# Kernel tuning notes

Hardware: AMD Instinct MI355X
Metric: run time of the kernel (lower is better)

The kernel has to match this reference:

```python
import jax, jax.numpy as jnp
import numpy as np

D_MODEL = 1024
N_HEADS = 16
SEQ = 512  # == max_seq_len; rel-pos bias requires n_token == max_seq_len


def setup_inputs() -> dict:
    key = jax.random.key(0)
    ks = jax.random.split(key, 12)
    B = 16
    x = jax.random.normal(ks[0], (B, SEQ, D_MODEL), dtype=jnp.float32)
    c = jax.random.normal(ks[1], (B, SEQ, 8), dtype=jnp.float32)  # unused by forward
    s = 1.0 / np.sqrt(D_MODEL)
    Wq = jax.random.normal(ks[2], (D_MODEL, D_MODEL), dtype=jnp.float32) * s
    bq = jnp.zeros((D_MODEL,), dtype=jnp.float32)
    Wk = jax.random.normal(ks[3], (D_MODEL, D_MODEL), dtype=jnp.float32) * s
    bk = jnp.zeros((D_MODEL,), dtype=jnp.float32)
    Wv = jax.random.normal(ks[4], (D_MODEL, D_MODEL), dtype=jnp.float32) * s
    bv = jnp.zeros((D_MODEL,), dtype=jnp.float32)
    Wo = jax.random.normal(ks[5], (D_MODEL, D_MODEL), dtype=jnp.float32) * s
    bo = jnp.zeros((D_MODEL,), dtype=jnp.float32)
    # trunc_normal_(std=0.02) approximated by normal*0.02 (values stay small)
    rel_table = jax.random.normal(ks[6], (2 * SEQ - 1, N_HEADS), dtype=jnp.float32) * 0.02
    return {"x": x, "c": c, "Wq": Wq, "bq": bq, "Wk": Wk, "bk": bk,
            "Wv": Wv, "bv": bv, "Wo": Wo, "bo": bo, "rel_table": rel_table}


def reference(x, c, Wq, bq, Wk, bk, Wv, bv, Wo, bo, rel_table):
    # x: [B, S, D]; c is unused in the original forward
    B, S, D = x.shape
    H = N_HEADS
    dk = D // H
    scale = 1.0 / np.sqrt(dk)

    q = (x @ Wq + bq).reshape(B, S, H, dk)
    k = (x @ Wk + bk).reshape(B, S, H, dk)
    v = (x @ Wv + bv).reshape(B, S, H, dk)

    # scores: [B, H, S, S]
    scores = jnp.einsum('bihd,bjhd->bhij', q, k) * scale

    # relative position bias: index[i,j] = i + (S-1-j), values in [0, 2S-2]
    rel_index = jnp.arange(S)[:, None] + jnp.arange(S - 1, -1, -1)[None, :]  # [S,S]
    bias = rel_table[rel_index]            # [S, S, H]
    scores = scores + jnp.transpose(bias, (2, 0, 1))[None]  # [1,H,S,S]

    # causal_mask=False: original adds False * -1e9 == 0, so no mask term
    probs = jax.nn.softmax(scores, axis=-1)

    out = jnp.einsum('bhij,bjhd->bihd', probs, v).reshape(B, S, D)
    return out @ Wo + bo
```

## Files before the change

### kernel.cpp

```cpp
#include <hip/hip_runtime.h>
#include <hip/hip_bf16.h>
#include <stdint.h>

#define D_MODEL 1024
#define NH 16
#define SEQ 512
#define DK 64
#define BATCH 16
#define M_TOT (BATCH*SEQ)

typedef unsigned short u16;
typedef unsigned int u32;
typedef __attribute__((ext_vector_type(8))) __bf16 bf16x8;
typedef __attribute__((ext_vector_type(4))) u16 ushort4v;
typedef __attribute__((ext_vector_type(4))) float f32x4;

static __device__ __forceinline__ u16 f2bf(float f) {
    union { float f; u32 i; } c; c.f = f;
    return (u16)((c.i + 0x8000u) >> 16);
}
static __device__ __forceinline__ void async_copy16(const void* g, void* l) {
    __builtin_amdgcn_global_load_lds(
        (const __attribute__((address_space(1))) u32*)g,
        (__attribute__((address_space(3))) u32*)l, 16, 0, 0);
}

__global__ __launch_bounds__(256) void convert_f32_bf16(const float* __restrict__ in,
                                                        u16* __restrict__ out) {
    const int i = (blockIdx.x * 256 + threadIdx.x) * 4;
    float4 v = *(const float4*)&in[i];
    ushort4v o;
    o[0] = f2bf(v.x); o[1] = f2bf(v.y); o[2] = f2bf(v.z); o[3] = f2bf(v.w);
    *(ushort4v*)&out[i] = o;
}

__global__ __launch_bounds__(256) void transpose_w3(const float* __restrict__ W0,
                                                    const float* __restrict__ W1,
                                                    const float* __restrict__ W2,
                                                    u16* __restrict__ Wt) {
    __shared__ u16 tile[64][65];
    const int z = blockIdx.z;
    const float* W = (z == 0) ? W0 : (z == 1) ? W1 : W2;
    const int n0 = blockIdx.x * 64, k0 = blockIdx.y * 64;
    const int t = threadIdx.x;
    #pragma unroll
    for (int p = 0; p < 16; ++p) {
        int idx = p * 256 + t;
        int r = idx >> 6, c = idx & 63;
        tile[r][c] = f2bf(W[(size_t)(k0 + r) * D_MODEL + (n0 + c)]);
    }
    __syncthreads();
    #pragma unroll
    for (int p = 0; p < 16; ++p) {
        int idx = p * 256 + t;
        int r = idx >> 6, c = idx & 63;
        Wt[((size_t)z * D_MODEL + n0 + r) * D_MODEL + (k0 + c)] = tile[c][r];
    }
}

__global__ __launch_bounds__(256) void gemm_bt(const u16* __restrict__ A,
                                               const u16* __restrict__ Bt,
                                               const float* __restrict__ b0,
                                               const float* __restrict__ b1,
                                               const float* __restrict__ b2,
                                               void* __restrict__ o0,
                                               void* __restrict__ o1,
                                               void* __restrict__ o2,
                                               int qkv) {
    __shared__ __attribute__((aligned(16))) u16 smem[16896];
    u16* Asm = smem;
    u16* Bsm = smem + 8192;
    const int t = threadIdx.x;
    const int m0 = blockIdx.y * 128, n0 = blockIdx.x * 128;
    const int lane = t & 63, w = t >> 6;
    const int lm = lane & 15, quad = lane >> 4;
    const int wm = w >> 1, wn = w & 1;

    f32x4 acc[4][4];
    #pragma unroll
    for (int i = 0; i < 4; ++i)
        #pragma unroll
        for (int j = 0; j < 4; ++j) acc[i][j] = (f32x4){0.f, 0.f, 0.f, 0.f};

    for (int kt = 0; kt < D_MODEL / 64; ++kt) {
        const int k0 = kt * 64;
        __syncthreads();
        #pragma unroll
        for (int i = 0; i < 4; ++i) {
            int chunk = i * 256 + t;
            int row = chunk >> 3, c = chunk & 7;
            int cs = c ^ (row & 7);
            async_copy16(A + (size_t)(m0 + row) * D_MODEL + k0 + cs * 8, &Asm[chunk * 8]);
        }
        #pragma unroll
        for (int i = 0; i < 4; ++i) {
            int chunk = i * 256 + t;
            int row = chunk >> 3, c = chunk & 7;
            int cs = c ^ (row & 7);
            async_copy16(Bt + (size_t)(n0 + row) * D_MODEL + k0 + cs * 8, &Bsm[chunk * 8]);
        }
        __syncthreads();
        #pragma unroll
        for (int ks = 0; ks < 64; ks += 32) {
            const int cbase = ks >> 3;
            bf16x8 af[4], bfv[4];
            #pragma unroll
            for (int im = 0; im < 4; ++im) {
                const int row = wm * 64 + im * 16 + lm;
                const int c = (cbase + quad) ^ (row & 7);
                af[im] = *(const bf16x8*)&Asm[row * 64 + c * 8];
            }
            #pragma unroll
            for (int in = 0; in < 4; ++in) {
                const int row = wn * 64 + in * 16 + lm;
                const int c = (cbase + quad) ^ (row & 7);
                bfv[in] = *(const bf16x8*)&Bsm[row * 64 + c * 8];
            }
            #pragma unroll
            for (int im = 0; im < 4; ++im)
                #pragma unroll
                for (int in = 0; in < 4; ++in)
                    acc[im][in] = __builtin_amdgcn_mfma_f32_16x16x32_bf16(
                        af[im], bfv[in], acc[im][in], 0, 0, 0);
        }
    }

    __syncthreads();
    if (qkv) {
        const int sel = n0 >> 10;
        if (sel == 2) {
            #pragma unroll
            for (int in = 0; in < 4; ++in) {
                const int nn = (n0 & 1023) + wn * 64 + in * 16 + lm;
                const float bv = b2[nn];
                const int h = nn >> 6, d = nn & 63;
                #pragma unroll
                for (int im = 0; im < 4; ++im) {
                    const int mb = m0 + wm * 64 + im * 16 + quad * 4;
                    const int b = mb >> 9, s = mb & 511;
                    ushort4v pk;
                    #pragma unroll
                    for (int r = 0; r < 4; ++r) pk[r] = f2bf(acc[im][in][r] + bv);
                    *(ushort4v*)&((u16*)o2)[((size_t)(b * NH + h) * DK + d) * SEQ + s] = pk;
                }
            }
        } else {
            u16* dst = sel ? (u16*)o1 : (u16*)o0;
            const float* bb = sel ? b1 : b0;
            u16 (*Cs)[132] = (u16(*)[132])smem;
            #pragma unroll
            for (int in = 0; in < 4; ++in) {
                const int nl = wn * 64 + in * 16 + lm;
                const float bv = bb[(n0 & 1023) + nl];
                #pragma unroll
                for (int im = 0; im < 4; ++im)
                    #pragma unroll
                    for (int r = 0; r < 4; ++r)
                        Cs[wm * 64 + im * 16 + quad * 4 + r][nl] =
                            f2bf(acc[im][in][r] + bv);
            }
            __syncthreads();
            const int rr = t >> 1, hh = t & 1;
            const int m = m0 + rr;
            const int b = m >> 9, s = m & 511;
            const int h = ((n0 & 1023) >> 6) + hh;
            u16* dp = &dst[((size_t)(b * NH + h) * SEQ + s) * DK];
            #pragma unroll
            for (int c = 0; c < 8; ++c)
                *(uint4*)&dp[c * 8] = *(const uint4*)&Cs[rr][hh * 64 + c * 8];
        }
    } else {
        float (*Cs)[132] = (float(*)[132])smem;
        #pragma unroll
        for (int ph = 0; ph < 2; ++ph) {
            if (wm == ph) {
                #pragma unroll
                for (int in = 0; in < 4; ++in) {
                    const int nl = wn * 64 + in * 16 + lm;
                    const float bv = b0[n0 + nl];
                    #pragma unroll
                    for (int im = 0; im < 4; ++im)
                        #pragma unroll
                        for (int r = 0; r < 4; ++r)
                            Cs[im * 16 + quad * 4 + r][nl] = acc[im][in][r] + bv;
                }
            }
            __syncthreads();
            const int rr = t >> 2, qq = t & 3;
            float* dp = &((float*)o0)[(size_t)(m0 + ph * 64 + rr) * D_MODEL + n0 + qq * 32];
            #pragma unroll
            for (int c = 0; c < 8; ++c)
                *(uint4*)&dp[c * 4] = *(const uint4*)&Cs[rr][qq * 32 + c * 4];
            __syncthreads();
        }
    }
}

__global__ __launch_bounds__(256) void attn_flash(const u16* __restrict__ qg,
                                                  const u16* __restrict__ kg,
                                                  const u16* __restrict__ vTg,
                                                  const float* __restrict__ rel,
                                                  u16* __restrict__ aout) {
    __shared__ __attribute__((aligned(16))) u16 qt[64 * 64];
    __shared__ __attribute__((aligned(16))) u16 kt[2][64 * 64];
    __shared__ __attribute__((aligned(16))) u16 vt[2][64 * 64];
    __shared__ __attribute__((aligned(16))) u16 Pl[4][16][72];
    __shared__ float biasb[576];

    const int t = threadIdx.x;
    const int lane = t & 63, w = t >> 6;
    const int lm = lane & 15, quad = lane >> 4;
    const int F = blockIdx.x;
    const int xcd = F & 7, qti = (F >> 3) & 7, grp = F >> 6;
    const int p = grp * 8 + xcd;
    const int h = p & 15, b = p >> 4;
    const int q0 = qti * 64;
    const size_t bh = (size_t)(b * NH + h);
    const u16* qb = qg + bh * SEQ * DK;
    const u16* kb = kg + bh * SEQ * DK;
    const u16* vb = vTg + bh * DK * SEQ;

    #pragma unroll
    for (int i = 0; i < 2; ++i) {
        const int chunk = i * 256 + t, row = chunk >> 3, c = chunk & 7;
        const int cs = c ^ (row & 7);
        *(uint4*)&qt[chunk * 8] = *(const uint4*)&qb[(q0 + row) * DK + cs * 8];
    }
    for (int u = t; u < 575; u += 256) biasb[u] = rel[(q0 + u) * NH + h];

    #pragma unroll
    for (int i = 0; i < 2; ++i) {
        const int chunk = i * 256 + t, row = chunk >> 3, c = chunk & 7;
        const int cs = c ^ (row & 7);
        async_copy16(kb + row * DK + cs * 8, &kt[0][chunk * 8]);
        async_copy16(vb + row * SEQ + cs * 8, &vt[0][chunk * 8]);
    }

    float lsum = 0.f;
    f32x4 o[4];
    #pragma unroll
    for (int sd = 0; sd < 4; ++sd) o[sd] = (f32x4){0.f, 0.f, 0.f, 0.f};

    const float scale = 0.125f;

    for (int jt = 0; jt < 8; ++jt) {
        __syncthreads();
        const int cur = jt & 1, nxt = cur ^ 1;
        if (jt < 7) {
            const int j1 = (jt + 1) * 64;
            #pragma unroll
            for (int i = 0; i < 2; ++i) {
                const int chunk = i * 256 + t, row = chunk >> 3, c = chunk & 7;
                const int cs = c ^ (row & 7);
                async_copy16(kb + (j1 + row) * DK + cs * 8, &kt[nxt][chunk * 8]);
                async_copy16(vb + row * SEQ + j1 + cs * 8, &vt[nxt][chunk * 8]);
            }
        }
        const int j0 = jt * 64;

        const int ra = w * 16 + lm;
        bf16x8 aq0 = *(const bf16x8*)&qt[ra * 64 + ((quad) ^ (ra & 7)) * 8];
        bf16x8 aq1 = *(const bf16x8*)&qt[ra * 64 + ((4 + quad) ^ (ra & 7)) * 8];
        #pragma unroll
        for (int js = 0; js < 4; ++js) {
            const int rb = js * 16 + lm;
            bf16x8 bk0 = *(const bf16x8*)&kt[cur][rb * 64 + ((quad) ^ (rb & 7)) * 8];
            bf16x8 bk1 = *(const bf16x8*)&kt[cur][rb * 64 + ((4 + quad) ^ (rb & 7)) * 8];
            f32x4 c = (f32x4){0.f, 0.f, 0.f, 0.f};
            c = __builtin_amdgcn_mfma_f32_16x16x32_bf16(bk0, aq0, c, 0, 0, 0);
            c = __builtin_amdgcn_mfma_f32_16x16x32_bf16(bk1, aq1, c, 0, 0, 0);
            const int bb0 = w * 16 + lm + 511 - j0 - js * 16 - quad * 4;
            ushort4v pk;
            #pragma unroll
            for (int r = 0; r < 4; ++r) {
                float e = __expf(c[r] * scale + biasb[bb0 - r]);
                lsum += e;
                pk[r] = f2bf(e);
            }
            *(ushort4v*)&Pl[w][lm][js * 16 + quad * 4] = pk;
        }

        bf16x8 ap0 = *(const bf16x8*)&Pl[w][lm][quad * 8];
        bf16x8 ap1 = *(const bf16x8*)&Pl[w][lm][32 + quad * 8];
        #pragma unroll
        for (int sd = 0; sd < 4; ++sd) {
            const int rv = sd * 16 + lm;
            bf16x8 bv0 = *(const bf16x8*)&vt[cur][rv * 64 + ((quad) ^ (rv & 7)) * 8];
            bf16x8 bv1 = *(const bf16x8*)&vt[cur][rv * 64 + ((4 + quad) ^ (rv & 7)) * 8];
            o[sd] = __builtin_amdgcn_mfma_f32_16x16x32_bf16(bv0, ap0, o[sd], 0, 0, 0);
            o[sd] = __builtin_amdgcn_mfma_f32_16x16x32_bf16(bv1, ap1, o[sd], 0, 0, 0);
        }
    }

    float s = lsum;
    s += __shfl_xor(s, 16, 64);
    s += __shfl_xor(s, 32, 64);
    const float rinv = 1.0f / s;
    #pragma unroll
    for (int sd = 0; sd < 4; ++sd) {
        ushort4v pk;
        #pragma unroll
        for (int r = 0; r < 4; ++r) pk[r] = f2bf(o[sd][r] * rinv);
        *(ushort4v*)&Pl[w][lm][sd * 16 + quad * 4] = pk;
    }
    const int rowl = lane >> 2, ch = lane & 3;
    u16* dp = aout + (size_t)(b * SEQ + q0 + w * 16 + rowl) * D_MODEL + h * DK + ch * 16;
    *(uint4*)&dp[0] = *(const uint4*)&Pl[w][rowl][ch * 16];
    *(uint4*)&dp[8] = *(const uint4*)&Pl[w][rowl][ch * 16 + 8];
}

extern "C" void kernel_launch(void* const* d_in, const int* in_sizes, int n_in,
                              void* d_out, int out_size, void* d_ws, size_t ws_size,
                              hipStream_t stream) {
    const float* x   = (const float*)d_in[0];
    const float* Wq  = (const float*)d_in[2];
    const float* bq  = (const float*)d_in[3];
    const float* Wk  = (const float*)d_in[4];
    const float* bk  = (const float*)d_in[5];
    const float* Wv  = (const float*)d_in[6];
    const float* bv  = (const float*)d_in[7];
    const float* Wo  = (const float*)d_in[8];
    const float* bo  = (const float*)d_in[9];
    const float* rel = (const float*)d_in[10];
    float* out = (float*)d_out;

    u16* ws = (u16*)d_ws;
    const size_t WSZ = (size_t)D_MODEL * D_MODEL;
    const size_t TSZ = (size_t)M_TOT * D_MODEL;
    u16* Wt3 = ws;
    u16* xbf = Wt3 + 3 * WSZ;
    u16* qws = xbf + TSZ;
    u16* kws = qws + TSZ;
    u16* vws = kws + TSZ;
    u16* aws = xbf;

    dim3 tb(256);
    convert_f32_bf16<<<dim3(M_TOT * D_MODEL / 1024), tb, 0, stream>>>(x, xbf);
    transpose_w3<<<dim3(16, 16, 3), tb, 0, stream>>>(Wq, Wk, Wv, Wt3);
    gemm_bt<<<dim3(24, 64), tb, 0, stream>>>(xbf, Wt3, bq, bk, bv, qws, kws, vws, 1);
    attn_flash<<<dim3(2048), tb, 0, stream>>>(qws, kws, vws, rel, aws);
    transpose_w3<<<dim3(16, 16, 1), tb, 0, stream>>>(Wo, Wo, Wo, Wt3);
    gemm_bt<<<dim3(8, 64), tb, 0, stream>>>(aws, Wt3, bo, nullptr, nullptr,
                                            (void*)out, nullptr, nullptr, 0);
}
```

Before: 258.0 us.

## Process 128 query rows per attention block and split QKV GEMM launch

The attention kernel now handles 128 query rows per block, two 16-row groups per wave, so each K/V tile loaded into shared memory feeds twice as many MFMAs. The grid is halved to 1024 blocks. This adds registers and LDS per block, which may lower occupancy. The fused QKV GEMM is also split into three launches of 8 column blocks each, using a new column-block offset argument, which adds launch overhead and possibly changes cache behaviour.

```diff
diff --git a/kernel.cpp b/kernel.cpp
--- a/kernel.cpp
+++ b/kernel.cpp
@@ -66,12 +66,12 @@
                                                void* __restrict__ o0,
                                                void* __restrict__ o1,
                                                void* __restrict__ o2,
-                                               int qkv) {
+                                               int qkv, int nb) {
     __shared__ __attribute__((aligned(16))) u16 smem[16896];
     u16* Asm = smem;
     u16* Bsm = smem + 8192;
     const int t = threadIdx.x;
-    const int m0 = blockIdx.y * 128, n0 = blockIdx.x * 128;
+    const int m0 = blockIdx.y * 128, n0 = (blockIdx.x + nb) * 128;
     const int lane = t & 63, w = t >> 6;
     const int lm = lane & 15, quad = lane >> 4;
     const int wm = w >> 1, wn = w & 1;
@@ -201,32 +201,32 @@
                                                   const u16* __restrict__ vTg,
                                                   const float* __restrict__ rel,
                                                   u16* __restrict__ aout) {
-    __shared__ __attribute__((aligned(16))) u16 qt[64 * 64];
+    __shared__ __attribute__((aligned(16))) u16 qt[128 * 64];
     __shared__ __attribute__((aligned(16))) u16 kt[2][64 * 64];
     __shared__ __attribute__((aligned(16))) u16 vt[2][64 * 64];
-    __shared__ __attribute__((aligned(16))) u16 Pl[4][16][72];
-    __shared__ float biasb[576];
+    __shared__ __attribute__((aligned(16))) u16 Pl[4][32][72];
+    __shared__ float biasb[640];
 
     const int t = threadIdx.x;
     const int lane = t & 63, w = t >> 6;
     const int lm = lane & 15, quad = lane >> 4;
     const int F = blockIdx.x;
-    const int xcd = F & 7, qti = (F >> 3) & 7, grp = F >> 6;
+    const int xcd = F & 7, qti = (F >> 3) & 3, grp = F >> 5;
     const int p = grp * 8 + xcd;
     const int h = p & 15, b = p >> 4;
-    const int q0 = qti * 64;
+    const int q0 = qti * 128;
     const size_t bh = (size_t)(b * NH + h);
     const u16* qb = qg + bh * SEQ * DK;
     const u16* kb = kg + bh * SEQ * DK;
     const u16* vb = vTg + bh * DK * SEQ;
 
     #pragma unroll
-    for (int i = 0; i < 2; ++i) {
+    for (int i = 0; i < 4; ++i) {
         const int chunk = i * 256 + t, row = chunk >> 3, c = chunk & 7;
         const int cs = c ^ (row & 7);
         *(uint4*)&qt[chunk * 8] = *(const uint4*)&qb[(q0 + row) * DK + cs * 8];
     }
-    for (int u = t; u < 575; u += 256) biasb[u] = rel[(q0 + u) * NH + h];
+    for (int u = t; u < 639; u += 256) biasb[u] = rel[(q0 + u) * NH + h];
 
     #pragma unroll
     for (int i = 0; i < 2; ++i) {
@@ -236,10 +236,12 @@
         async_copy16(vb + row * SEQ + cs * 8, &vt[0][chunk * 8]);
     }
 
-    float lsum = 0.f;
-    f32x4 o[4];
-    #pragma unroll
-    for (int sd = 0; sd < 4; ++sd) o[sd] = (f32x4){0.f, 0.f, 0.f, 0.f};
+    float lsum[2] = {0.f, 0.f};
+    f32x4 o[2][4];
+    #pragma unroll
+    for (int g = 0; g < 2; ++g)
+        #pragma unroll
+        for (int sd = 0; sd < 4; ++sd) o[g][sd] = (f32x4){0.f, 0.f, 0.f, 0.f};
 
     const float scale = 0.125f;
 
@@ -258,55 +260,73 @@
         }
         const int j0 = jt * 64;
 
-        const int ra = w * 16 + lm;
-        bf16x8 aq0 = *(const bf16x8*)&qt[ra * 64 + ((quad) ^ (ra & 7)) * 8];
-        bf16x8 aq1 = *(const bf16x8*)&qt[ra * 64 + ((4 + quad) ^ (ra & 7)) * 8];
+        bf16x8 aq[2][2];
+        #pragma unroll
+        for (int g = 0; g < 2; ++g) {
+            const int ra = w * 32 + g * 16 + lm;
+            aq[g][0] = *(const bf16x8*)&qt[ra * 64 + ((quad) ^ (ra & 7)) * 8];
+            aq[g][1] = *(const bf16x8*)&qt[ra * 64 + ((4 + quad) ^ (ra & 7)) * 8];
+        }
         #pragma unroll
         for (int js = 0; js < 4; ++js) {
             const int rb = js * 16 + lm;
             bf16x8 bk0 = *(const bf16x8*)&kt[cur][rb * 64 + ((quad) ^ (rb & 7)) * 8];
             bf16x8 bk1 = *(const bf16x8*)&kt[cur][rb * 64 + ((4 + quad) ^ (rb & 7)) * 8];
-            f32x4 c = (f32x4){0.f, 0.f, 0.f, 0.f};
-            c = __builtin_amdgcn_mfma_f32_16x16x32_bf16(bk0, aq0, c, 0, 0, 0);
-            c = __builtin_amdgcn_mfma_f32_16x16x32_bf16(bk1, aq1, c, 0, 0, 0);
-            const int bb0 = w * 16 + lm + 511 - j0 - js * 16 - quad * 4;
-            ushort4v pk;
-            #pragma unroll
-            for (int r = 0; r < 4; ++r) {
-                float e = __expf(c[r] * scale + biasb[bb0 - r]);
-                lsum += e;
-                pk[r] = f2bf(e);
-            }
-            *(ushort4v*)&Pl[w][lm][js * 16 + quad * 4] = pk;
-        }
-
-        bf16x8 ap0 = *(const bf16x8*)&Pl[w][lm][quad * 8];
-        bf16x8 ap1 = *(const bf16x8*)&Pl[w][lm][32 + quad * 8];
+            #pragma unroll
+            for (int g = 0; g < 2; ++g) {
+                f32x4 c = (f32x4){0.f, 0.f, 0.f, 0.f};
+                c = __builtin_amdgcn_mfma_f32_16x16x32_bf16(bk0, aq[g][0], c, 0, 0, 0);
+                c = __builtin_amdgcn_mfma_f32_16x16x32_bf16(bk1, aq[g][1], c, 0, 0, 0);
+                const int bb0 = w * 32 + g * 16 + lm + 511 - j0 - js * 16 - quad * 4;
+                ushort4v pk;
+                #pragma unroll
+                for (int r = 0; r < 4; ++r) {
+                    float e = __expf(c[r] * scale + biasb[bb0 - r]);
+                    lsum[g] += e;
+                    pk[r] = f2bf(e);
+                }
+                *(ushort4v*)&Pl[w][g * 16 + lm][js * 16 + quad * 4] = pk;
+            }
+        }
+
+        bf16x8 ap[2][2];
+        #pragma unroll
+        for (int g = 0; g < 2; ++g) {
+            ap[g][0] = *(const bf16x8*)&Pl[w][g * 16 + lm][quad * 8];
+            ap[g][1] = *(const bf16x8*)&Pl[w][g * 16 + lm][32 + quad * 8];
+        }
         #pragma unroll
         for (int sd = 0; sd < 4; ++sd) {
             const int rv = sd * 16 + lm;
             bf16x8 bv0 = *(const bf16x8*)&vt[cur][rv * 64 + ((quad) ^ (rv & 7)) * 8];
             bf16x8 bv1 = *(const bf16x8*)&vt[cur][rv * 64 + ((4 + quad) ^ (rv & 7)) * 8];
-            o[sd] = __builtin_amdgcn_mfma_f32_16x16x32_bf16(bv0, ap0, o[sd], 0, 0, 0);
-            o[sd] = __builtin_amdgcn_mfma_f32_16x16x32_bf16(bv1, ap1, o[sd], 0, 0, 0);
-        }
-    }
-
-    float s = lsum;
-    s += __shfl_xor(s, 16, 64);
-    s += __shfl_xor(s, 32, 64);
-    const float rinv = 1.0f / s;
-    #pragma unroll
-    for (int sd = 0; sd < 4; ++sd) {
-        ushort4v pk;
-        #pragma unroll
-        for (int r = 0; r < 4; ++r) pk[r] = f2bf(o[sd][r] * rinv);
-        *(ushort4v*)&Pl[w][lm][sd * 16 + quad * 4] = pk;
-    }
-    const int rowl = lane >> 2, ch = lane & 3;
-    u16* dp = aout + (size_t)(b * SEQ + q0 + w * 16 + rowl) * D_MODEL + h * DK + ch * 16;
-    *(uint4*)&dp[0] = *(const uint4*)&Pl[w][rowl][ch * 16];
-    *(uint4*)&dp[8] = *(const uint4*)&Pl[w][rowl][ch * 16 + 8];
+            #pragma unroll
+            for (int g = 0; g < 2; ++g) {
+                o[g][sd] = __builtin_amdgcn_mfma_f32_16x16x32_bf16(bv0, ap[g][0], o[g][sd], 0, 0, 0);
+                o[g][sd] = __builtin_amdgcn_mfma_f32_16x16x32_bf16(bv1, ap[g][1], o[g][sd], 0, 0, 0);
+            }
+        }
+    }
+
+    #pragma unroll
+    for (int g = 0; g < 2; ++g) {
+        float s = lsum[g];
+        s += __shfl_xor(s, 16, 64);
+        s += __shfl_xor(s, 32, 64);
+        const float rinv = 1.0f / s;
+        #pragma unroll
+        for (int sd = 0; sd < 4; ++sd) {
+            ushort4v pk;
+            #pragma unroll
+            for (int r = 0; r < 4; ++r) pk[r] = f2bf(o[g][sd][r] * rinv);
+            *(ushort4v*)&Pl[w][g * 16 + lm][sd * 16 + quad * 4] = pk;
+        }
+    }
+    const int rowl = lane >> 1, ch = lane & 1;
+    u16* dp = aout + (size_t)(b * SEQ + q0 + w * 32 + rowl) * D_MODEL + h * DK + ch * 32;
+    #pragma unroll
+    for (int c = 0; c < 4; ++c)
+        *(uint4*)&dp[c * 8] = *(const uint4*)&Pl[w][rowl][ch * 32 + c * 8];
 }
 
 extern "C" void kernel_launch(void* const* d_in, const int* in_sizes, int n_in,
@@ -337,9 +357,11 @@
     dim3 tb(256);
     convert_f32_bf16<<<dim3(M_TOT * D_MODEL / 1024), tb, 0, stream>>>(x, xbf);
     transpose_w3<<<dim3(16, 16, 3), tb, 0, stream>>>(Wq, Wk, Wv, Wt3);
-    gemm_bt<<<dim3(24, 64), tb, 0, stream>>>(xbf, Wt3, bq, bk, bv, qws, kws, vws, 1);
-    attn_flash<<<dim3(2048), tb, 0, stream>>>(qws, kws, vws, rel, aws);
+    gemm_bt<<<dim3(8, 64), tb, 0, stream>>>(xbf, Wt3, bq, bk, bv, qws, kws, vws, 1, 0);
+    gemm_bt<<<dim3(8, 64), tb, 0, stream>>>(xbf, Wt3, bq, bk, bv, qws, kws, vws, 1, 8);
+    gemm_bt<<<dim3(8, 64), tb, 0, stream>>>(xbf, Wt3, bq, bk, bv, qws, kws, vws, 1, 16);
+    attn_flash<<<dim3(1024), tb, 0, stream>>>(qws, kws, vws, rel, aws);
     transpose_w3<<<dim3(16, 16, 1), tb, 0, stream>>>(Wo, Wo, Wo, Wt3);
     gemm_bt<<<dim3(8, 64), tb, 0, stream>>>(aws, Wt3, bo, nullptr, nullptr,
-                                            (void*)out, nullptr, nullptr, 0);
-}
+                                            (void*)out, nullptr, nullptr, 0, 0);
+}
```

Result: slower. 270.7 us (+4.9%).
